# Kernel tuning notes

Measured on AMD Instinct MI355X. Metric: run time of the kernel, lower is better.

The kernel has to match this reference:

```python
import jax, jax.numpy as jnp
import numpy as np

V, E, H, B, S = 50257, 1024, 1024, 32, 1024

def setup_inputs() -> dict:
    key = jax.random.key(0)
    ks = jax.random.split(key, 16)
    s = 0.02
    return {
        "word_inputs": jax.random.randint(ks[0], (B, 1), 0, V),
        "hidden": jax.random.normal(ks[1], (1, B, H), jnp.float32),
        "output_encoder": jax.random.normal(ks[2], (B, S, H), jnp.float32),
        "emb": jax.random.normal(ks[3], (V, E), jnp.float32) * 0.2,
        "W_a1": jax.random.normal(ks[4], (H, 2 * H), jnp.float32) * s,
        "b_a1": jnp.zeros((H,), jnp.float32),
        "W_a2": jax.random.normal(ks[5], (1, H), jnp.float32) * s,
        "b_a2": jnp.zeros((1,), jnp.float32),
        "W_c": jax.random.normal(ks[6], (H, 2 * H), jnp.float32) * s,
        "b_c": jnp.zeros((H,), jnp.float32),
        "W_ih": jax.random.normal(ks[7], (3 * H, E), jnp.float32) * s,
        "W_hh": jax.random.normal(ks[8], (3 * H, H), jnp.float32) * s,
        "b_ih": jnp.zeros((3 * H,), jnp.float32),
        "b_hh": jnp.zeros((3 * H,), jnp.float32),
        "W_fc": jax.random.normal(ks[9], (V, H), jnp.float32) * 0.2,
        "b_fc": jnp.zeros((V,), jnp.float32),
    }

def reference(word_inputs, hidden, output_encoder, emb, W_a1, b_a1, W_a2, b_a2,
              W_c, b_c, W_ih, W_hh, b_ih, b_hh, W_fc, b_fc):
    b, s, h = output_encoder.shape
    h_prev = hidden[0]                                      # [B,H]
    # Bahdanau additive attention, vectorized over all S timesteps
    eh = jnp.concatenate(
        [output_encoder, jnp.broadcast_to(h_prev[:, None, :], (b, s, h))],
        axis=-1)                                            # [B,S,2H]
    scores = jnp.tanh(jnp.einsum('bsk,hk->bsh', eh, W_a1) + b_a1)
    scores = (jnp.einsum('bsh,oh->bso', scores, W_a2) + b_a2)[..., 0]  # [B,S]
    attn = jax.nn.softmax(scores, axis=1)                   # [B,S]
    context = jnp.einsum('bs,bsh->bh', attn, output_encoder)  # [B,H]
    embedded = emb[word_inputs.reshape(-1)]                 # [B,E]
    ec = jnp.concatenate([embedded, context], axis=-1)      # [B,E+H]
    x = jax.nn.relu(ec @ W_c.T + b_c)                       # [B,H]
    # single-step GRU (PyTorch gate order: r, z, n)
    gi = x @ W_ih.T + b_ih                                  # [B,3H]
    gh = h_prev @ W_hh.T + b_hh                             # [B,3H]
    i_r, i_z, i_n = jnp.split(gi, 3, axis=-1)
    h_r, h_z, h_n = jnp.split(gh, 3, axis=-1)
    r = jax.nn.sigmoid(i_r + h_r)
    z = jax.nn.sigmoid(i_z + h_z)
    n = jnp.tanh(i_n + r * h_n)
    h_new = (1.0 - z) * n + z * h_prev                      # [B,H]
    out = jax.nn.relu(h_new) @ W_fc.T + b_fc                # [B,V]
    return out, h_new[None, :, :]
```

## Files before the change

### kernel.cpp

```cpp
#include <hip/hip_runtime.h>

#define B_  32
#define S_  1024
#define H_  1024
#define V_  50257

typedef __attribute__((ext_vector_type(8))) short bf16x8;
typedef __attribute__((ext_vector_type(4))) float f32x4;
typedef __attribute__((ext_vector_type(8))) unsigned short u16x8;

__device__ __forceinline__ unsigned short f2b(float f) {
  union { float f; unsigned u; } v; v.f = f;
  unsigned r = 0x7FFFu + ((v.u >> 16) & 1u);
  return (unsigned short)((v.u + r) >> 16);
}
__device__ __forceinline__ float b2f(unsigned short h) {
  union { unsigned u; float f; } v; v.u = ((unsigned)h) << 16;
  return v.f;
}

__device__ __forceinline__ void async16(void* lds, const void* g) {
  typedef __attribute__((address_space(3))) void as3_void;
  typedef __attribute__((address_space(1))) void as1_void;
  as3_void* l = (as3_void*)(unsigned)(unsigned long long)lds;
  const as1_void* s = (const as1_void*)(unsigned long long)g;
  __builtin_amdgcn_global_load_lds(s, l, 16, 0, 0);
}

__global__ void prologue_kernel(const float* __restrict__ enc, unsigned short* __restrict__ enc_bf,
                                const float* __restrict__ wa1, const float* __restrict__ hidden,
                                const float* __restrict__ b_a1,
                                unsigned short* __restrict__ wa1_bf, float* __restrict__ part2) {
  __shared__ float wrow[H_];
  int tid = threadIdx.x;
  if (blockIdx.x < 16384) {
    size_t i = ((size_t)blockIdx.x * 256 + tid) * 8;
    float4 v0 = *(const float4*)(enc + i);
    float4 v1 = *(const float4*)(enc + i + 4);
    u16x8 o;
    o[0]=f2b(v0.x); o[1]=f2b(v0.y); o[2]=f2b(v0.z); o[3]=f2b(v0.w);
    o[4]=f2b(v1.x); o[5]=f2b(v1.y); o[6]=f2b(v1.z); o[7]=f2b(v1.w);
    *(u16x8*)(enc_bf + i) = o;
    return;
  }
  int h = blockIdx.x - 16384;
  {
    int c = tid * 4;
    float4 v = *(const float4*)(wa1 + (size_t)h * 2048 + c);
    ushort4 o;
    o.x = f2b(v.x); o.y = f2b(v.y); o.z = f2b(v.z); o.w = f2b(v.w);
    *(ushort4*)(wa1_bf + (size_t)h * 1024 + c) = o;
  }
  {
    int c = tid * 4;
    float4 v = *(const float4*)(wa1 + (size_t)h * 2048 + 1024 + c);
    wrow[c] = v.x; wrow[c+1] = v.y; wrow[c+2] = v.z; wrow[c+3] = v.w;
  }
  __syncthreads();
  int wave = tid >> 6, lane = tid & 63;
  float bias = b_a1[h];
  for (int bb = 0; bb < 8; ++bb) {
    int b = wave * 8 + bb;
    float acc = 0.f;
    for (int k = lane; k < H_; k += 64) acc += wrow[k] * hidden[b * H_ + k];
    #pragma unroll
    for (int off = 32; off; off >>= 1) acc += __shfl_xor(acc, off);
    if (lane == 0) part2[b * H_ + h] = acc + bias;
  }
}

__global__ __launch_bounds__(256) void scores_m97(
    const unsigned short* __restrict__ A,
    const unsigned short* __restrict__ Bm,
    const float* __restrict__ part2,
    const float* __restrict__ wa2,
    float* __restrict__ partials)
{
  __shared__ __align__(16) unsigned short As[4096];
  __shared__ __align__(16) unsigned short Bs[4096];
  const int tid = threadIdx.x;
  const int wave = tid >> 6, lane = tid & 63;
  const int wr = wave >> 1, wc = wave & 1;
  const int l15 = lane & 15, l16 = lane >> 4;
  const int bn = blockIdx.x, bm = blockIdx.y;

  const unsigned short* Abase = A  + (size_t)(bm * 128) * 1024;
  const unsigned short* Bbase = Bm + (size_t)(bn * 128) * 1024;

  const int Lc = tid * 16;
  const int r0 = Lc >> 6;
  const int cb0 = (Lc & 63) ^ (((r0 >> 1) & 3) << 4);
  const int ce0 = cb0 >> 1;

  f32x4 acc[4][4];
  #pragma unroll
  for (int mi = 0; mi < 4; ++mi)
    #pragma unroll
    for (int ni = 0; ni < 4; ++ni) acc[mi][ni] = (f32x4){0.f, 0.f, 0.f, 0.f};
  bf16x8 af[4], bfr[4];

  for (int kt = 0; kt < 1024; kt += 32) {
    async16((char*)As + Lc,        Abase + (size_t)r0 * 1024 + kt + ce0);
    async16((char*)As + Lc + 4096, Abase + (size_t)(r0 + 64) * 1024 + kt + ce0);
    async16((char*)Bs + Lc,        Bbase + (size_t)r0 * 1024 + kt + ce0);
    async16((char*)Bs + Lc + 4096, Bbase + (size_t)(r0 + 64) * 1024 + kt + ce0);
    asm volatile("s_waitcnt vmcnt(0)" ::: "memory");
    __syncthreads();
    #pragma unroll
    for (int mi = 0; mi < 4; ++mi) {
      int ar = wr * 64 + mi * 16 + l15;
      int L = ar * 64 + l16 * 16;
      af[mi] = *(const bf16x8*)((const char*)As + (L ^ (((ar >> 1) & 3) << 4)));
    }
    #pragma unroll
    for (int ni = 0; ni < 4; ++ni) {
      int br = wc * 64 + ni * 16 + l15;
      int L = br * 64 + l16 * 16;
      bfr[ni] = *(const bf16x8*)((const char*)Bs + (L ^ (((br >> 1) & 3) << 4)));
    }
    #pragma unroll
    for (int mi = 0; mi < 4; ++mi)
      #pragma unroll
      for (int ni = 0; ni < 4; ++ni)
        acc[mi][ni] = __builtin_amdgcn_mfma_f32_16x16x32_bf16(af[mi], bfr[ni], acc[mi][ni], 0, 0, 0);
    __syncthreads();
  }

  const int b = bm >> 3;
  float w2[4], p2[4];
  #pragma unroll
  for (int ni = 0; ni < 4; ++ni) {
    int col = bn * 128 + wc * 64 + ni * 16 + l15;
    w2[ni] = wa2[col];
    p2[ni] = part2[b * H_ + col];
  }
  #pragma unroll
  for (int mi = 0; mi < 4; ++mi) {
    #pragma unroll
    for (int r = 0; r < 4; ++r) {
      float s = 0.f;
      #pragma unroll
      for (int ni = 0; ni < 4; ++ni)
        s += w2[ni] * tanhf(acc[mi][ni][r] + p2[ni]);
      s += __shfl_xor(s, 1); s += __shfl_xor(s, 2);
      s += __shfl_xor(s, 4); s += __shfl_xor(s, 8);
      if (l15 == 0) {
        int row = bm * 128 + wr * 64 + mi * 16 + l16 * 4 + r;
        partials[(size_t)row * 16 + bn * 2 + wc] = s;
      }
    }
  }
}

__global__ __launch_bounds__(256) void smctx_kernel(
    const float* __restrict__ partials, const unsigned short* __restrict__ encbf,
    float* __restrict__ ctxp) {
  int sc = blockIdx.x, b = blockIdx.y, tid = threadIdx.x;
  int lane = tid & 63, wid = tid >> 6;
  __shared__ float att[1024];
  __shared__ float red[4];
  float scv[4];
  float mx = -1e30f;
  #pragma unroll
  for (int j = 0; j < 4; ++j) {
    int r = tid * 4 + j;
    const float4* p = (const float4*)(partials + ((size_t)b * 1024 + r) * 16);
    float s = 0.f;
    #pragma unroll
    for (int i = 0; i < 4; ++i) { float4 v = p[i]; s += v.x + v.y + v.z + v.w; }
    scv[j] = s; mx = fmaxf(mx, s);
  }
  #pragma unroll
  for (int off = 32; off; off >>= 1) mx = fmaxf(mx, __shfl_xor(mx, off));
  if (lane == 0) red[wid] = mx;
  __syncthreads();
  float M = fmaxf(fmaxf(red[0], red[1]), fmaxf(red[2], red[3]));
  float ssum = 0.f;
  #pragma unroll
  for (int j = 0; j < 4; ++j) { float e = expf(scv[j] - M); att[tid*4+j] = e; ssum += e; }
  #pragma unroll
  for (int off = 32; off; off >>= 1) ssum += __shfl_xor(ssum, off);
  __syncthreads();
  if (lane == 0) red[wid] = ssum;
  __syncthreads();
  float inv = 1.f / (red[0] + red[1] + red[2] + red[3]);
  int h4 = tid * 4;
  float a0 = 0, a1 = 0, a2 = 0, a3 = 0;
  const unsigned short* base = encbf + (size_t)b * S_ * H_ + h4;
  #pragma unroll 4
  for (int i = 0; i < 64; ++i) {
    float w = att[sc * 64 + i] * inv;
    ushort4 ev = *(const ushort4*)(base + (size_t)(sc * 64 + i) * H_);
    a0 += w * b2f(ev.x); a1 += w * b2f(ev.y); a2 += w * b2f(ev.z); a3 += w * b2f(ev.w);
  }
  float4 o = {a0, a1, a2, a3};
  *(float4*)(ctxp + (size_t)(sc * B_ + b) * H_ + h4) = o;
}

__global__ __launch_bounds__(256) void wc_gemm(
    const int* __restrict__ word, const float* __restrict__ emb,
    const float* __restrict__ ctxp, const float* __restrict__ Wc,
    float* __restrict__ xp) {
  int nb = blockIdx.x, kc = blockIdx.y, tid = threadIdx.x;
  __shared__ unsigned short A_lds[32][136];
  {
    int b = tid >> 3, cg = tid & 7;
    int c0 = cg * 16;
    if (kc < 8) {
      int w = word[b];
      const float* er = emb + (size_t)w * H_ + kc * 128 + c0;
      #pragma unroll
      for (int c = 0; c < 16; c += 4) {
        float4 v = *(const float4*)(er + c);
        ushort4 o; o.x = f2b(v.x); o.y = f2b(v.y); o.z = f2b(v.z); o.w = f2b(v.w);
        *(ushort4*)&A_lds[b][c0 + c] = o;
      }
    } else {
      int h0 = (kc - 8) * 128 + c0;
      #pragma unroll
      for (int c = 0; c < 16; c += 4) {
        float s0 = 0, s1 = 0, s2 = 0, s3 = 0;
        #pragma unroll
        for (int sc = 0; sc < 16; ++sc) {
          float4 v = *(const float4*)(ctxp + ((size_t)(sc * B_ + b)) * H_ + h0 + c);
          s0 += v.x; s1 += v.y; s2 += v.z; s3 += v.w;
        }
        ushort4 o; o.x = f2b(s0); o.y = f2b(s1); o.z = f2b(s2); o.w = f2b(s3);
        *(ushort4*)&A_lds[b][c0 + c] = o;
      }
    }
  }
  __syncthreads();
  int wave = tid >> 6, lane = tid & 63, l15 = lane & 15, l16 = lane >> 4;
  int col = nb * 64 + wave * 16 + l15;
  const float* bp = Wc + (size_t)col * 2048 + kc * 128 + l16 * 8;
  f32x4 acc0 = {0.f,0.f,0.f,0.f}, acc1 = {0.f,0.f,0.f,0.f};
  #pragma unroll
  for (int k = 0; k < 128; k += 32) {
    bf16x8 a0 = *(const bf16x8*)&A_lds[l15][k + l16 * 8];
    bf16x8 a1 = *(const bf16x8*)&A_lds[16 + l15][k + l16 * 8];
    float4 bv0 = *(const float4*)(bp + k);
    float4 bv1 = *(const float4*)(bp + k + 4);
    bf16x8 bb;
    bb[0] = (short)f2b(bv0.x); bb[1] = (short)f2b(bv0.y);
    bb[2] = (short)f2b(bv0.z); bb[3] = (short)f2b(bv0.w);
    bb[4] = (short)f2b(bv1.x); bb[5] = (short)f2b(bv1.y);
    bb[6] = (short)f2b(bv1.z); bb[7] = (short)f2b(bv1.w);
    acc0 = __builtin_amdgcn_mfma_f32_16x16x32_bf16(a0, bb, acc0, 0, 0, 0);
    acc1 = __builtin_amdgcn_mfma_f32_16x16x32_bf16(a1, bb, acc1, 0, 0, 0);
  }
  #pragma unroll
  for (int r = 0; r < 4; ++r) {
    int m = l16 * 4 + r;
    xp[(size_t)(kc * 32 + m) * H_ + col] = acc0[r];
    xp[(size_t)(kc * 32 + 16 + m) * H_ + col] = acc1[r];
  }
}

__global__ __launch_bounds__(256) void ihhh_gemm(
    const float* __restrict__ xp, const float* __restrict__ b_c,
    const float* __restrict__ hidden,
    const float* __restrict__ W_ih, const float* __restrict__ W_hh,
    float* __restrict__ gip, float* __restrict__ ghp) {
  int nb = blockIdx.x, kc = blockIdx.y, z = blockIdx.z, tid = threadIdx.x;
  __shared__ unsigned short A_lds[32][136];
  {
    int b = tid >> 3, cg = tid & 7;
    int c0 = cg * 16;
    int h0 = kc * 128 + c0;
    if (z == 0) {
      #pragma unroll
      for (int c = 0; c < 16; c += 4) {
        float4 bias = *(const float4*)(b_c + h0 + c);
        float s0 = bias.x, s1 = bias.y, s2 = bias.z, s3 = bias.w;
        #pragma unroll
        for (int sc = 0; sc < 16; ++sc) {
          float4 v = *(const float4*)(xp + ((size_t)(sc * B_ + b)) * H_ + h0 + c);
          s0 += v.x; s1 += v.y; s2 += v.z; s3 += v.w;
        }
        ushort4 o;
        o.x = f2b(fmaxf(s0, 0.f)); o.y = f2b(fmaxf(s1, 0.f));
        o.z = f2b(fmaxf(s2, 0.f)); o.w = f2b(fmaxf(s3, 0.f));
        *(ushort4*)&A_lds[b][c0 + c] = o;
      }
    } else {
      #pragma unroll
      for (int c = 0; c < 16; c += 4) {
        float4 v = *(const float4*)(hidden + (size_t)b * H_ + h0 + c);
        ushort4 o; o.x = f2b(v.x); o.y = f2b(v.y); o.z = f2b(v.z); o.w = f2b(v.w);
        *(ushort4*)&A_lds[b][c0 + c] = o;
      }
    }
  }
  __syncthreads();
  const float* Bw = z ? W_hh : W_ih;
  float* C = z ? ghp : gip;
  int wave = tid >> 6, lane = tid & 63, l15 = lane & 15, l16 = lane >> 4;
  int col = nb * 64 + wave * 16 + l15;
  const float* bp = Bw + (size_t)col * 1024 + kc * 128 + l16 * 8;
  f32x4 acc0 = {0.f,0.f,0.f,0.f}, acc1 = {0.f,0.f,0.f,0.f};
  #pragma unroll
  for (int k = 0; k < 128; k += 32) {
    bf16x8 a0 = *(const bf16x8*)&A_lds[l15][k + l16 * 8];
    bf16x8 a1 = *(const bf16x8*)&A_lds[16 + l15][k + l16 * 8];
    float4 bv0 = *(const float4*)(bp + k);
    float4 bv1 = *(const float4*)(bp + k + 4);
    bf16x8 bb;
    bb[0] = (short)f2b(bv0.x); bb[1] = (short)f2b(bv0.y);
    bb[2] = (short)f2b(bv0.z); bb[3] = (short)f2b(bv0.w);
    bb[4] = (short)f2b(bv1.x); bb[5] = (short)f2b(bv1.y);
    bb[6] = (short)f2b(bv1.z); bb[7] = (short)f2b(bv1.w);
    acc0 = __builtin_amdgcn_mfma_f32_16x16x32_bf16(a0, bb, acc0, 0, 0, 0);
    acc1 = __builtin_amdgcn_mfma_f32_16x16x32_bf16(a1, bb, acc1, 0, 0, 0);
  }
  #pragma unroll
  for (int r = 0; r < 4; ++r) {
    int m = l16 * 4 + r;
    C[(size_t)(kc * 32 + m) * 3072 + col] = acc0[r];
    C[(size_t)(kc * 32 + 16 + m) * 3072 + col] = acc1[r];
  }
}

__global__ void gates_kernel(const float* __restrict__ gip, const float* __restrict__ ghp,
                             const float* __restrict__ b_ih, const float* __restrict__ b_hh,
                             const float* __restrict__ hidden, float* __restrict__ hnew_out,
                             unsigned short* __restrict__ hr_bf) {
  int i = blockIdx.x * 256 + threadIdx.x;
  int b = i >> 10, h = i & 1023;
  float g[6];
  #pragma unroll
  for (int t = 0; t < 3; ++t) {
    int j = h + t * H_;
    float vi = b_ih[j], vh = b_hh[j];
    #pragma unroll
    for (int kc = 0; kc < 8; ++kc) {
      vi += gip[(size_t)(kc * B_ + b) * 3072 + j];
      vh += ghp[(size_t)(kc * B_ + b) * 3072 + j];
    }
    g[t] = vi; g[3 + t] = vh;
  }
  float r = 1.f / (1.f + expf(-(g[0] + g[3])));
  float z = 1.f / (1.f + expf(-(g[1] + g[4])));
  float n = tanhf(g[2] + r * g[5]);
  float hv = (1.f - z) * n + z * hidden[i];
  hnew_out[i] = hv;
  hr_bf[i] = f2b(hv > 0.f ? hv : 0.f);
}

__global__ __launch_bounds__(256) void fc_gemm(
    const unsigned short* __restrict__ A, const float* __restrict__ Bw,
    float* __restrict__ C, const float* __restrict__ bias) {
  const int N = V_, K = 1024;
  int n0 = blockIdx.x * 64;
  int wave = threadIdx.x >> 6, lane = threadIdx.x & 63;
  int l15 = lane & 15, l16 = lane >> 4;
  int col = n0 + wave * 16 + l15;
  int vclamp = col < N ? col : N - 1;
  const unsigned short* a0p = A + l15 * K + l16 * 8;
  const unsigned short* a1p = A + (16 + l15) * K + l16 * 8;
  const float* bp = Bw + (size_t)vclamp * K + l16 * 8;
  f32x4 acc0 = {0.f,0.f,0.f,0.f}, acc1 = {0.f,0.f,0.f,0.f};
  #pragma unroll 4
  for (int k = 0; k < K; k += 32) {
    bf16x8 a0 = *(const bf16x8*)(a0p + k);
    bf16x8 a1 = *(const bf16x8*)(a1p + k);
    float4 bv0 = *(const float4*)(bp + k);
    float4 bv1 = *(const float4*)(bp + k + 4);
    bf16x8 bb;
    bb[0] = (short)f2b(bv0.x); bb[1] = (short)f2b(bv0.y);
    bb[2] = (short)f2b(bv0.z); bb[3] = (short)f2b(bv0.w);
    bb[4] = (short)f2b(bv1.x); bb[5] = (short)f2b(bv1.y);
    bb[6] = (short)f2b(bv1.z); bb[7] = (short)f2b(bv1.w);
    acc0 = __builtin_amdgcn_mfma_f32_16x16x32_bf16(a0, bb, acc0, 0, 0, 0);
    acc1 = __builtin_amdgcn_mfma_f32_16x16x32_bf16(a1, bb, acc1, 0, 0, 0);
  }
  if (col < N) {
    float bv = bias[col];
    #pragma unroll
    for (int r = 0; r < 4; ++r) {
      int m = l16 * 4 + r;
      C[(size_t)m * N + col] = acc0[r] + bv;
      C[(size_t)(16 + m) * N + col] = acc1[r] + bv;
    }
  }
}

extern "C" void kernel_launch(void* const* d_in, const int* in_sizes, int n_in,
                              void* d_out, int out_size, void* d_ws, size_t ws_size,
                              hipStream_t stream) {
  const int*   word   = (const int*)  d_in[0];
  const float* hidden = (const float*)d_in[1];
  const float* enc    = (const float*)d_in[2];
  const float* emb    = (const float*)d_in[3];
  const float* W_a1   = (const float*)d_in[4];
  const float* b_a1   = (const float*)d_in[5];
  const float* W_a2   = (const float*)d_in[6];
  const float* b_c    = (const float*)d_in[9];
  const float* W_c    = (const float*)d_in[8];
  const float* W_ih   = (const float*)d_in[10];
  const float* W_hh   = (const float*)d_in[11];
  const float* b_ih   = (const float*)d_in[12];
  const float* b_hh   = (const float*)d_in[13];
  const float* W_fc   = (const float*)d_in[14];
  const float* b_fc   = (const float*)d_in[15];
  float* out = (float*)d_out;

  if (ws_size < 73596928ull) return;

  char* ws = (char*)d_ws;
  unsigned short* enc_bf   = (unsigned short*)(ws + 0);
  float*          gip      = (float*)         (ws + 0);
  float*          ghp      = (float*)         (ws + 3145728);
  unsigned short* wa1_bf   = (unsigned short*)(ws + 67108864);
  float*          xp       = (float*)         (ws + 67108864);
  float*          part2    = (float*)         (ws + 69206016);
  float*          partials = (float*)         (ws + 69337088);
  float*          ctxp     = (float*)         (ws + 71434240);
  unsigned short* hr_bf    = (unsigned short*)(ws + 73531392);

  prologue_kernel<<<dim3(17408), dim3(256), 0, stream>>>(enc, enc_bf, W_a1, hidden, b_a1,
                                                         wa1_bf, part2);
  scores_m97<<<dim3(8, 256), dim3(256), 0, stream>>>(enc_bf, wa1_bf, part2, W_a2, partials);
  smctx_kernel<<<dim3(16, 32), dim3(256), 0, stream>>>(partials, enc_bf, ctxp);
  wc_gemm<<<dim3(16, 16), dim3(256), 0, stream>>>(word, emb, ctxp, W_c, xp);
  ihhh_gemm<<<dim3(48, 8, 2), dim3(256), 0, stream>>>(xp, b_c, hidden, W_ih, W_hh, gip, ghp);
  gates_kernel<<<dim3(128), dim3(256), 0, stream>>>(gip, ghp, b_ih, b_hh, hidden,
                                                    out + (size_t)B_ * V_, hr_bf);
  fc_gemm<<<dim3(786), dim3(256), 0, stream>>>(hr_bf, W_fc, out, b_fc);
}
```

Measured before the change: 300.4 us.

## Load MFMA fragments directly from global memory with register double-buffering

Rewrites the attention-score GEMM so each wave loads its bf16 fragments straight from global memory into registers, dropping the LDS staging, XOR swizzle and both per-iteration barriers. A two-stage register ping-pong overlaps the next K-slice's loads with the current MFMAs. This removes sync and LDS traffic, but each wave now re-reads operands the other waves also read, so data reuse shifts to L1/L2. The global accesses are 16-byte chunks per lane with a 2KB row stride, which coalesce poorly.

```diff
diff --git a/kernel.cpp b/kernel.cpp
--- a/kernel.cpp
+++ b/kernel.cpp
@@ -69,62 +69,55 @@
   }
 }
 
-__global__ __launch_bounds__(256) void scores_m97(
+#define LDF(AV, BV, KT) { \
+  _Pragma("unroll") for (int mi = 0; mi < 4; ++mi) AV[mi] = *(const bf16x8*)(ap[mi] + (KT)); \
+  _Pragma("unroll") for (int ni = 0; ni < 4; ++ni) BV[ni] = *(const bf16x8*)(bp[ni] + (KT)); }
+
+#define FMAQ(AV, BV) { \
+  _Pragma("unroll") for (int mi = 0; mi < 4; ++mi) \
+    _Pragma("unroll") for (int ni = 0; ni < 4; ++ni) \
+      acc[mi][ni] = __builtin_amdgcn_mfma_f32_16x16x32_bf16(AV[mi], BV[ni], acc[mi][ni], 0, 0, 0); }
+
+__global__ __launch_bounds__(256) void scores_nolds(
     const unsigned short* __restrict__ A,
     const unsigned short* __restrict__ Bm,
     const float* __restrict__ part2,
     const float* __restrict__ wa2,
     float* __restrict__ partials)
 {
-  __shared__ __align__(16) unsigned short As[4096];
-  __shared__ __align__(16) unsigned short Bs[4096];
   const int tid = threadIdx.x;
   const int wave = tid >> 6, lane = tid & 63;
   const int wr = wave >> 1, wc = wave & 1;
   const int l15 = lane & 15, l16 = lane >> 4;
   const int bn = blockIdx.x, bm = blockIdx.y;
 
-  const unsigned short* Abase = A  + (size_t)(bm * 128) * 1024;
-  const unsigned short* Bbase = Bm + (size_t)(bn * 128) * 1024;
-
-  const int Lc = tid * 16;
-  const int r0 = Lc >> 6;
-  const int cb0 = (Lc & 63) ^ (((r0 >> 1) & 3) << 4);
-  const int ce0 = cb0 >> 1;
+  const unsigned short* ap[4];
+  const unsigned short* bp[4];
+  #pragma unroll
+  for (int mi = 0; mi < 4; ++mi)
+    ap[mi] = A + (size_t)(bm * 128 + wr * 64 + mi * 16 + l15) * 1024 + l16 * 8;
+  #pragma unroll
+  for (int ni = 0; ni < 4; ++ni)
+    bp[ni] = Bm + (size_t)(bn * 128 + wc * 64 + ni * 16 + l15) * 1024 + l16 * 8;
 
   f32x4 acc[4][4];
   #pragma unroll
   for (int mi = 0; mi < 4; ++mi)
     #pragma unroll
     for (int ni = 0; ni < 4; ++ni) acc[mi][ni] = (f32x4){0.f, 0.f, 0.f, 0.f};
-  bf16x8 af[4], bfr[4];
-
-  for (int kt = 0; kt < 1024; kt += 32) {
-    async16((char*)As + Lc,        Abase + (size_t)r0 * 1024 + kt + ce0);
-    async16((char*)As + Lc + 4096, Abase + (size_t)(r0 + 64) * 1024 + kt + ce0);
-    async16((char*)Bs + Lc,        Bbase + (size_t)r0 * 1024 + kt + ce0);
-    async16((char*)Bs + Lc + 4096, Bbase + (size_t)(r0 + 64) * 1024 + kt + ce0);
-    asm volatile("s_waitcnt vmcnt(0)" ::: "memory");
-    __syncthreads();
-    #pragma unroll
-    for (int mi = 0; mi < 4; ++mi) {
-      int ar = wr * 64 + mi * 16 + l15;
-      int L = ar * 64 + l16 * 16;
-      af[mi] = *(const bf16x8*)((const char*)As + (L ^ (((ar >> 1) & 3) << 4)));
-    }
-    #pragma unroll
-    for (int ni = 0; ni < 4; ++ni) {
-      int br = wc * 64 + ni * 16 + l15;
-      int L = br * 64 + l16 * 16;
-      bfr[ni] = *(const bf16x8*)((const char*)Bs + (L ^ (((br >> 1) & 3) << 4)));
-    }
-    #pragma unroll
-    for (int mi = 0; mi < 4; ++mi)
-      #pragma unroll
-      for (int ni = 0; ni < 4; ++ni)
-        acc[mi][ni] = __builtin_amdgcn_mfma_f32_16x16x32_bf16(af[mi], bfr[ni], acc[mi][ni], 0, 0, 0);
-    __syncthreads();
-  }
+
+  bf16x8 a0[4], b0[4], a1[4], b1[4];
+  LDF(a0, b0, 0);
+  #pragma unroll 1
+  for (int kt = 0; kt < 960; kt += 64) {
+    LDF(a1, b1, kt + 32);
+    FMAQ(a0, b0);
+    LDF(a0, b0, kt + 64);
+    FMAQ(a1, b1);
+  }
+  LDF(a1, b1, 992);
+  FMAQ(a0, b0);
+  FMAQ(a1, b1);
 
   const int b = bm >> 3;
   float w2[4], p2[4];
@@ -420,7 +413,7 @@
 
   prologue_kernel<<<dim3(17408), dim3(256), 0, stream>>>(enc, enc_bf, W_a1, hidden, b_a1,
                                                          wa1_bf, part2);
-  scores_m97<<<dim3(8, 256), dim3(256), 0, stream>>>(enc_bf, wa1_bf, part2, W_a2, partials);
+  scores_nolds<<<dim3(8, 256), dim3(256), 0, stream>>>(enc_bf, wa1_bf, part2, W_a2, partials);
   smctx_kernel<<<dim3(16, 32), dim3(256), 0, stream>>>(partials, enc_bf, ctxp);
   wc_gemm<<<dim3(16, 16), dim3(256), 0, stream>>>(word, emb, ctxp, W_c, xp);
   ihhh_gemm<<<dim3(48, 8, 2), dim3(256), 0, stream>>>(xp, b_c, hidden, W_ih, W_hh, gip, ghp);
```

New measurement: 449.5 us. 1.5x slower.
